# Optimization experiments

Measured on AMD Instinct MI355X. Metric: run time of the kernel, lower is better.

## Reference

```python
import jax, jax.numpy as jnp
import numpy as np

B, T, D, H, K = 128, 64, 2048, 512, 512
WINDOWS = [2, 3, 4]
ROUT = 2 * H            # bidirectional GRU output dim = 1024
FIN = ROUT + len(WINDOWS) * K + 2048 + 1024  # 5632 ('full' concat)
FOUT = 2048
BN_EPS = 1e-5


def setup_inputs() -> dict:
    key = jax.random.key(0)
    ks = jax.random.split(key, 32)
    s = 0.02
    inp = {
        "videos": jax.random.normal(ks[0], (B, T, D), jnp.float32),
        "motions": jax.random.normal(ks[1], (B, 1024), jnp.float32),
        "videos_origin": jax.random.normal(ks[2], (B, 2048), jnp.float32),
        "lengths": jax.random.randint(ks[3], (B,), 1, T + 1, jnp.int32),
        # GRU params (PyTorch layout: gates ordered r,z,n stacked on dim 0)
        "Wih_f": jax.random.normal(ks[4], (3 * H, D), jnp.float32) * s,
        "Whh_f": jax.random.normal(ks[5], (3 * H, H), jnp.float32) * s,
        "bih_f": jnp.zeros((3 * H,), jnp.float32),
        "bhh_f": jnp.zeros((3 * H,), jnp.float32),
        "Wih_b": jax.random.normal(ks[6], (3 * H, D), jnp.float32) * s,
        "Whh_b": jax.random.normal(ks[7], (3 * H, H), jnp.float32) * s,
        "bih_b": jnp.zeros((3 * H,), jnp.float32),
        "bhh_b": jnp.zeros((3 * H,), jnp.float32),
        # FC + BatchNorm1d (eval-mode) of MFC
        "fc_w": jax.random.normal(ks[8], (FOUT, FIN), jnp.float32) * (np.sqrt(6.0) / np.sqrt(FIN + FOUT)),
        "fc_b": jnp.zeros((FOUT,), jnp.float32),
        "bn_gamma": jnp.ones((FOUT,), jnp.float32),
        "bn_beta": jnp.zeros((FOUT,), jnp.float32),
        "bn_mean": jnp.zeros((FOUT,), jnp.float32),
        "bn_var": jnp.ones((FOUT,), jnp.float32),
    }
    for i, ws in enumerate(WINDOWS):
        inp[f"conv_w{ws}"] = jax.random.normal(ks[10 + 2 * i], (K, 1, ws, ROUT), jnp.float32) * s
        inp[f"conv_b{ws}"] = jnp.zeros((K,), jnp.float32)
    # mask consistent with lengths: mask[b,t] = t < lengths[b]
    inp["videos_mask"] = (jnp.arange(T)[None, :] < inp["lengths"][:, None]).astype(jnp.float32)
    return inp


def _gru_dir(x, Wih, Whh, bih, bhh, reverse):
    # x: [B,T,D] -> outputs [B,T,H]; torch GRU cell with r,z,n gate order
    xg = jnp.einsum("btd,gd->btg", x, Wih) + bih  # [B,T,3H] precomputed input gates

    def step(h, xg_t):
        hg = h @ Whh.T + bhh
        xr, xz, xn = jnp.split(xg_t, 3, axis=-1)
        hr, hz, hn = jnp.split(hg, 3, axis=-1)
        r = jax.nn.sigmoid(xr + hr)
        z = jax.nn.sigmoid(xz + hz)
        n = jnp.tanh(xn + r * hn)
        h_new = (1.0 - z) * n + z * h
        return h_new, h_new

    h0 = jnp.zeros((x.shape[0], Whh.shape[1]), x.dtype)
    _, hs = jax.lax.scan(step, h0, jnp.swapaxes(xg, 0, 1), reverse=reverse)
    return jnp.swapaxes(hs, 0, 1)


def _conv_branch(x4, w, b, ws):
    # x4: [B,1,T,ROUT], w: [K,1,ws,ROUT]; torch padding=(ws-1, 0)
    y = jax.lax.conv_general_dilated(
        x4, w, (1, 1), [(ws - 1, ws - 1), (0, 0)],
        dimension_numbers=("NCHW", "OIHW", "NCHW"))  # [B,K,T+ws-1,1]
    y = jax.nn.relu(y + b[None, :, None, None])
    return jnp.max(y, axis=(2, 3))  # max_pool1d over full time -> [B,K]


def _forward(videos, motions, videos_origin, lengths, videos_mask,
             Wih_f, Whh_f, bih_f, bhh_f, Wih_b, Whh_b, bih_b, bhh_b,
             conv_w2, conv_b2, conv_w3, conv_b3, conv_w4, conv_b4,
             fc_w, fc_b, bn_gamma, bn_beta, bn_mean, bn_var):
    fwd = _gru_dir(videos, Wih_f, Whh_f, bih_f, bhh_f, reverse=False)
    bwd = _gru_dir(videos, Wih_b, Whh_b, bih_b, bhh_b, reverse=True)
    gru_init_out = jnp.concatenate([fwd, bwd], axis=-1)  # [B,T,2H]

    # masked mean over valid frames (vectorized version of the batch for-loop)
    denom = lengths.astype(gru_init_out.dtype)[:, None]
    gru_out = jnp.sum(gru_init_out * videos_mask[:, :, None], axis=1) / denom  # [B,2H]

    masked = gru_init_out * videos_mask[:, :, None]
    x4 = masked[:, None, :, :]  # [B,1,T,2H]
    con_out = jnp.concatenate([
        _conv_branch(x4, conv_w2, conv_b2, 2),
        _conv_branch(x4, conv_w3, conv_b3, 3),
        _conv_branch(x4, conv_w4, conv_b4, 4),
    ], axis=1)  # [B,3K]

    # concate == 'full' (dropout is identity in eval)
    features = jnp.concatenate([gru_out, con_out, videos_origin, motions], axis=1)
    features = features @ fc_w.T + fc_b
    # BatchNorm1d, eval mode with running stats
    features = bn_gamma * (features - bn_mean) * jax.lax.rsqrt(bn_var + BN_EPS) + bn_beta
    # l2norm over dim 1
    features = features / jnp.sqrt(jnp.sum(features * features, axis=1, keepdims=True))
    return features


def reference(videos, motions, videos_origin, lengths, videos_mask,
              Wih_f, Whh_f, bih_f, bhh_f, Wih_b, Whh_b, bih_b, bhh_b,
              conv_w2, conv_b2, conv_w3, conv_b3, conv_w4, conv_b4,
              fc_w, fc_b, bn_gamma, bn_beta, bn_mean, bn_var):
    return _forward(videos, motions, videos_origin, lengths, videos_mask,
                    Wih_f, Whh_f, bih_f, bhh_f, Wih_b, Whh_b, bih_b, bhh_b,
                    conv_w2, conv_b2, conv_w3, conv_b3, conv_w4, conv_b4,
                    fc_w, fc_b, bn_gamma, bn_beta, bn_mean, bn_var)
```

## Files before the change

### kernel.cpp

```cpp
#include <hip/hip_runtime.h>
#include <hip/hip_bf16.h>
#include <stdint.h>

typedef __attribute__((ext_vector_type(8))) short short8;
typedef __attribute__((ext_vector_type(4))) float floatx4;
typedef __attribute__((ext_vector_type(4))) unsigned int u32x4;
typedef unsigned short u16;
typedef unsigned int u32;
typedef unsigned long long u64;

static __device__ __forceinline__ u16 f2bf(float f) {
  union { float f; u32 u; } v; v.f = f;
  return (u16)((v.u + 0x7fffu + ((v.u >> 16) & 1u)) >> 16);
}
static __device__ __forceinline__ float bf2f(u16 h) {
  union { u32 u; float f; } v; v.u = ((u32)h) << 16; return v.f;
}
static __device__ __forceinline__ u64 pack4(float a, float b, float c, float d) {
  return (u64)f2bf(a) | ((u64)f2bf(b) << 16) | ((u64)f2bf(c) << 32) | ((u64)f2bf(d) << 48);
}

__global__ __launch_bounds__(256) void k_pre_cvt(
    const float* __restrict__ videos, const float* __restrict__ Wih_f,
    const float* __restrict__ Wih_b, const float* __restrict__ Whh_f,
    const float* __restrict__ Whh_b, const float* __restrict__ bih_f,
    const float* __restrict__ bih_b, const float* __restrict__ fcb,
    const float* __restrict__ gam, const float* __restrict__ bet,
    const float* __restrict__ mu, const float* __restrict__ var,
    u16* __restrict__ vid, u16* __restrict__ wih, u16* __restrict__ whh,
    float* __restrict__ bihcat, float* __restrict__ bns, float* __restrict__ bnt)
{
  const int O1 = 4194304;
  const int O2 = O1 + 786432;
  const int O3 = O2 + 786432;
  const int O4 = O3 + 196608;
  const int O5 = O4 + 196608;
  const int NQ = O5 + 1280;
  for (int q = blockIdx.x * 256 + threadIdx.x; q < NQ; q += gridDim.x * 256) {
    if (q < O1) {
      float4 v = ((const float4*)videos)[q];
      ((u64*)vid)[q] = pack4(v.x, v.y, v.z, v.w);
    } else if (q < O2) {
      int r = q - O1; float4 v = ((const float4*)Wih_f)[r];
      ((u64*)wih)[r] = pack4(v.x, v.y, v.z, v.w);
    } else if (q < O3) {
      int r = q - O2; float4 v = ((const float4*)Wih_b)[r];
      ((u64*)wih)[r + 786432] = pack4(v.x, v.y, v.z, v.w);
    } else if (q < O4) {
      int r = q - O3; float4 v = ((const float4*)Whh_f)[r];
      ((u64*)whh)[r] = pack4(v.x, v.y, v.z, v.w);
    } else if (q < O5) {
      int r = q - O4; float4 v = ((const float4*)Whh_b)[r];
      ((u64*)whh)[r + 196608] = pack4(v.x, v.y, v.z, v.w);
    } else {
      int r = q - O5;
      if (r < 768) {
        int i = r * 4;
        const float* s = (i < 1536) ? (bih_f + i) : (bih_b + (i - 1536));
        *(float4*)&bihcat[i] = *(const float4*)s;
      } else {
        int i = (r - 768) * 4;
#pragma unroll
        for (int j = 0; j < 4; ++j) {
          int idx = i + j;
          float sc = gam[idx] * rsqrtf(var[idx] + 1e-5f);
          bns[idx] = sc;
          bnt[idx] = sc * (fcb[idx] - mu[idx]) + bet[idx];
        }
      }
    }
  }
}

static __device__ __forceinline__ void gload_lds16(const u16* g, u16* l) {
  __builtin_amdgcn_global_load_lds((const __attribute__((address_space(1))) u32*)(const void*)g,
                                   (__attribute__((address_space(3))) u32*)(void*)l, 16, 0, 0);
}

static __device__ __forceinline__ void stage_half_256(
    const u16* __restrict__ Mat, long K, int rowbase, int ktile, u16* lregion,
    int tid, int wid)
{
  int srow = tid >> 3;
  int sce = (((tid >> 3) ^ tid) & 7) * 8;
  const u16* g0 = Mat + (long)(rowbase + srow) * K + ktile * 64 + sce;
  const u16* g1 = Mat + (long)(rowbase + 64 + srow) * K + ktile * 64 + sce;
  gload_lds16(g0, lregion + wid * 512);
  gload_lds16(g1, lregion + 4096 + wid * 512);
}

__global__ __launch_bounds__(512) void gemm256(
    const u16* __restrict__ A, const u16* __restrict__ Bm,
    float* __restrict__ C, u16* __restrict__ C16, int M, int N, int K, int NT,
    const float* __restrict__ shift)
{
  __shared__ u16 lds[65536];
  int tid = threadIdx.x, lane = tid & 63, wid = tid >> 6;
  int r16 = lane & 15, kq = lane >> 4;
  int wr = wid >> 2, wc = wid & 3;
  int nwg = gridDim.x * gridDim.y;
  int lin = blockIdx.y * gridDim.x + blockIdx.x;
  int q8 = nwg >> 3;
  int swz = (lin & 7) * q8 + (lin >> 3);
  int m0 = (swz / gridDim.x) * 256, n0 = (swz % gridDim.x) * 256;

  int fxor = (r16 & 7) << 4;
  int c0 = (kq * 16) ^ fxor;
  int c1 = c0 ^ 64;
  int brow0 = (wc & 1) * 64;
  const char* ldsc = (const char*)lds;

  const floatx4 z4 = {0.f, 0.f, 0.f, 0.f};
  floatx4 acc[8][4];
#pragma unroll
  for (int i = 0; i < 8; ++i)
#pragma unroll
    for (int j = 0; j < 4; ++j) acc[i][j] = z4;

  stage_half_256(Bm, K, n0,       0, lds,                 tid, wid);
  stage_half_256(Bm, K, n0 + 128, 0, lds + 8192,          tid, wid);
  stage_half_256(A,  K, m0,       0, lds + 16384,         tid, wid);
  stage_half_256(A,  K, m0 + 128, 0, lds + 24576,         tid, wid);
  stage_half_256(Bm, K, n0,       1, lds + 32768,         tid, wid);
  stage_half_256(Bm, K, n0 + 128, 1, lds + 32768 + 8192,  tid, wid);
  stage_half_256(A,  K, m0,       1, lds + 32768 + 16384, tid, wid);
  stage_half_256(A,  K, m0 + 128, 1, lds + 32768 + 24576, tid, wid);
  asm volatile("s_waitcnt vmcnt(8)" ::: "memory");
  asm volatile("s_barrier" ::: "memory");

#define MFMA_CLUSTER(q)                                                        \
  asm volatile("s_waitcnt lgkmcnt(0)" ::: "memory");                           \
  __builtin_amdgcn_sched_barrier(0);                                           \
  __builtin_amdgcn_s_setprio(1);                                               \
  _Pragma("unroll")                                                            \
  for (int s = 0; s < 2; ++s)                                                  \
    _Pragma("unroll")                                                          \
    for (int e = 0; e < 2; ++e)                                                \
      _Pragma("unroll")                                                        \
      for (int j = 0; j < 4; ++j)                                              \
        acc[(q)*2 + e][j] = __builtin_amdgcn_mfma_f32_16x16x32_bf16(           \
            af[e][s], bf[j][s], acc[(q)*2 + e][j], 0, 0, 0);                   \
  __builtin_amdgcn_s_setprio(0);

  for (int T = 0; T < NT; ++T) {
    int P = T & 1;
    int Tn1 = (T + 1 < NT) ? T + 1 : 0;
    int Tn2 = (T + 2 < NT) ? T + 2 : T + 2 - NT;
    const char* bbase = ldsc + P * 65536 + (wc >> 1) * 16384;
    const char* abase = ldsc + P * 65536 + 32768 + wr * 16384;
    short8 bf[4][2];
    {
#pragma unroll
      for (int j = 0; j < 4; ++j) {
        bf[j][0] = *(const short8*)(bbase + (brow0 + j * 16 + r16) * 128 + c0);
        bf[j][1] = *(const short8*)(bbase + (brow0 + j * 16 + r16) * 128 + c1);
      }
      short8 af[2][2];
#pragma unroll
      for (int e = 0; e < 2; ++e) {
        af[e][0] = *(const short8*)(abase + (e * 16 + r16) * 128 + c0);
        af[e][1] = *(const short8*)(abase + (e * 16 + r16) * 128 + c1);
      }
      stage_half_256(A, K, m0, Tn1, lds + (Tn1 & 1) * 32768 + 16384, tid, wid);
      asm volatile("s_barrier" ::: "memory");
      MFMA_CLUSTER(0)
      asm volatile("s_barrier" ::: "memory");
    }
    {
      short8 af[2][2];
#pragma unroll
      for (int e = 0; e < 2; ++e) {
        af[e][0] = *(const short8*)(abase + ((2 + e) * 16 + r16) * 128 + c0);
        af[e][1] = *(const short8*)(abase + ((2 + e) * 16 + r16) * 128 + c1);
      }
      stage_half_256(A, K, m0 + 128, Tn1, lds + (Tn1 & 1) * 32768 + 24576, tid, wid);
      asm volatile("s_barrier" ::: "memory");
      MFMA_CLUSTER(1)
      asm volatile("s_barrier" ::: "memory");
    }
    {
      short8 af[2][2];
#pragma unroll
      for (int e = 0; e < 2; ++e) {
        af[e][0] = *(const short8*)(abase + ((4 + e) * 16 + r16) * 128 + c0);
        af[e][1] = *(const short8*)(abase + ((4 + e) * 16 + r16) * 128 + c1);
      }
      stage_half_256(Bm, K, n0, Tn2, lds + P * 32768, tid, wid);
      asm volatile("s_barrier" ::: "memory");
      MFMA_CLUSTER(2)
      asm volatile("s_barrier" ::: "memory");
    }
    {
      short8 af[2][2];
#pragma unroll
      for (int e = 0; e < 2; ++e) {
        af[e][0] = *(const short8*)(abase + ((6 + e) * 16 + r16) * 128 + c0);
        af[e][1] = *(const short8*)(abase + ((6 + e) * 16 + r16) * 128 + c1);
      }
      stage_half_256(Bm, K, n0 + 128, Tn2, lds + P * 32768 + 8192, tid, wid);
      asm volatile("s_barrier" ::: "memory");
      MFMA_CLUSTER(3)
      asm volatile("s_waitcnt vmcnt(4)" ::: "memory");
      asm volatile("s_barrier" ::: "memory");
    }
  }
#undef MFMA_CLUSTER

#pragma unroll
  for (int mf = 0; mf < 8; ++mf)
#pragma unroll
    for (int j = 0; j < 4; ++j) {
      int col = n0 + wc * 64 + j * 16 + r16;
      int row = m0 + wr * 128 + mf * 16 + kq * 4;
      if (C16) {
#pragma unroll
        for (int qq = 0; qq < 4; ++qq)
          C16[(long)(row + qq) * N + col] = f2bf(acc[mf][j][qq]);
      } else {
        float sh = shift ? shift[col] : 0.f;
#pragma unroll
        for (int qq = 0; qq < 4; ++qq)
          C[(long)(row + qq) * N + col] = acc[mf][j][qq] + sh;
      }
    }
}

__global__ __launch_bounds__(256) void gemm_bt(
    const u16* __restrict__ A, const u16* __restrict__ Bm,
    float* __restrict__ C, u16* __restrict__ C16, int M, int N, int K, int kn,
    const float* __restrict__ scale, const float* __restrict__ shift)
{
  __shared__ u16 As[128 * 32];
  __shared__ u16 Bs[128 * 32];
  int tid = threadIdx.x, lane = tid & 63, wid = tid >> 6;
  int nwg = gridDim.x * gridDim.y;
  int lin = blockIdx.y * gridDim.x + blockIdx.x;
  int q8 = nwg >> 3;
  int swz = (lin & 7) * q8 + (lin >> 3);
  int m0 = (swz / gridDim.x) * 128, n0 = (swz % gridDim.x) * 128;
  int kt0 = blockIdx.z * kn;
  int wr = wid >> 1, wc = wid & 1;
  int r16 = lane & 15, kq = lane >> 4;
  const floatx4 z4 = {0.f, 0.f, 0.f, 0.f};
  floatx4 acc[4][4];
#pragma unroll
  for (int i = 0; i < 4; ++i)
#pragma unroll
    for (int j = 0; j < 4; ++j) acc[i][j] = z4;
  for (int kt = kt0; kt < kt0 + kn; ++kt) {
    __syncthreads();
#pragma unroll
    for (int inst = 0; inst < 2; ++inst) {
      int g = inst * 256 + tid;
      int row = g >> 2, cb = g & 3;
      const u16* ga = A + (long)(m0 + row) * K + kt * 32 + cb * 8;
      const u16* gb = Bm + (long)(n0 + row) * K + kt * 32 + cb * 8;
      gload_lds16(ga, &As[(inst * 256 + wid * 64) * 8]);
      gload_lds16(gb, &Bs[(inst * 256 + wid * 64) * 8]);
    }
    __syncthreads();
    short8 af[4], bf[4];
#pragma unroll
    for (int mt = 0; mt < 4; ++mt) af[mt] = *(const short8*)&As[(wr * 64 + mt * 16 + r16) * 32 + kq * 8];
#pragma unroll
    for (int nt = 0; nt < 4; ++nt) bf[nt] = *(const short8*)&Bs[(wc * 64 + nt * 16 + r16) * 32 + kq * 8];
#pragma unroll
    for (int mt = 0; mt < 4; ++mt)
#pragma unroll
      for (int nt = 0; nt < 4; ++nt)
        acc[mt][nt] = __builtin_amdgcn_mfma_f32_16x16x32_bf16(af[mt], bf[nt], acc[mt][nt], 0, 0, 0);
  }
  float* Cp = C + (long)blockIdx.z * M * N;
#pragma unroll
  for (int nt = 0; nt < 4; ++nt) {
    int col = n0 + wc * 64 + nt * 16 + r16;
    float sc = scale ? scale[col] : 1.f;
    float sh = shift ? shift[col] : 0.f;
#pragma unroll
    for (int mt = 0; mt < 4; ++mt)
#pragma unroll
      for (int q = 0; q < 4; ++q) {
        int row = m0 + wr * 64 + mt * 16 + kq * 4 + q;
        float v = acc[mt][nt][q] * sc + sh;
        if (C16) C16[(long)row * N + col] = f2bf(v);
        else     Cp[(long)row * N + col] = v;
      }
  }
}

__global__ __launch_bounds__(512) void gru_rec(
    const float* __restrict__ xg,
    const u16* __restrict__ whhb,
    const float* __restrict__ bhh_f, const float* __restrict__ bhh_b,
    char* __restrict__ hb3,
    u16* __restrict__ maskb,
    u16* __restrict__ feat,
    const int* __restrict__ lengths,
    const float* __restrict__ fc_w, const float* __restrict__ w2,
    const float* __restrict__ w3, const float* __restrict__ w4,
    const float* __restrict__ vo, const float* __restrict__ mo,
    u16* __restrict__ fcw, u16* __restrict__ wc)
{
  __shared__ float part[2][4][3][256];
  __shared__ u16 hstage[8192];
  int tid = threadIdx.x, lane = tid & 63, wid = tid >> 6;
  int bid = blockIdx.x;

  if (bid >= 128) {
    int cid = bid - 128;
    const int C1 = 2883584;
    const int C2 = C1 + 1179648;
    const int C3 = C2 + 65536;
    const int NQ = C3 + 32768;
    for (int q = cid * 512 + tid; q < NQ; q += 128 * 512) {
      if (q < C1) {
        float4 v = ((const float4*)fc_w)[q];
        ((u64*)fcw)[q] = pack4(v.x, v.y, v.z, v.w);
      } else if (q < C2) {
        int r = q - C1;
        int e = r << 2;
        int row = e >> 10, col = e & 1023;
        const float* src;
        if (row < 1024)      { int j = row >> 9, k = row & 511;                 src = w2 + (k * 2 + j) * 1024; }
        else if (row < 2560) { int m = row - 1024; int j = m >> 9, k = m & 511; src = w3 + (k * 3 + j) * 1024; }
        else                 { int m = row - 2560; int j = m >> 9, k = m & 511; src = w4 + (k * 4 + j) * 1024; }
        float4 v = *(const float4*)(src + col);
        ((u64*)wc)[r] = pack4(v.x, v.y, v.z, v.w);
      } else if (q < C3) {
        int r = q - C2; int b = r >> 9, c = (r & 511) * 4;
        float4 v = *(const float4*)&vo[(long)b * 2048 + c];
        *(u64*)&feat[(long)b * 5632 + 2560 + c] = pack4(v.x, v.y, v.z, v.w);
      } else {
        int r = q - C3; int b = r >> 8, c = (r & 255) * 4;
        float4 v = *(const float4*)&mo[(long)b * 1024 + c];
        *(u64*)&feat[(long)b * 5632 + 4608 + c] = pack4(v.x, v.y, v.z, v.w);
      }
    }
    return;
  }

  int dir = bid >> 6, rem = bid & 63, bt = rem >> 3, is = rem & 7;
  int ih = wid & 3, ks = wid >> 2;
  int r16 = lane & 15, kq = lane >> 4;
  int iglob = is * 64 + ih * 16 + r16;
  int i0 = is * 64 + ih * 16 + kq * 4;
  int batch = bt * 16 + r16;
  const float* bhh = dir ? bhh_b : bhh_f;
  const floatx4 z4 = {0.f, 0.f, 0.f, 0.f};
  int len = lengths[batch];

  short8 wfrag[3][8];
#pragma unroll
  for (int g = 0; g < 3; ++g) {
    const u16* wrow = whhb + (long)(dir * 1536 + g * 512 + iglob) * 512;
#pragma unroll
    for (int kk = 0; kk < 8; ++kk)
      wfrag[g][kk] = *(const short8*)&wrow[(ks * 8 + kk) * 32 + kq * 8];
  }
  float4 bh4[3];
#pragma unroll
  for (int g = 0; g < 3; ++g) bh4[g] = *(const float4*)&bhh[g * 512 + i0];
  float4 hprev = {0.f, 0.f, 0.f, 0.f};
  float4 msum = {0.f, 0.f, 0.f, 0.f};

  float4 px[3];
  if (ks == 0) {
    int ts0 = dir ? 63 : 0;
    long xb = (long)(batch * 64 + ts0) * 3072 + dir * 1536 + i0;
#pragma unroll
    for (int g = 0; g < 3; ++g) px[g] = *(const float4*)&xg[xb + g * 512];
  }

  char* slot[2];
  slot[0] = hb3 + (long)((0 * 2 + dir) * 8 + bt) * 32768;
  slot[1] = hb3 + (long)((1 * 2 + dir) * 8 + bt) * 32768;
  char* sdst[4];
#pragma unroll
  for (int k = 0; k < 4; ++k) {
    int row = 4 * k + (tid >> 7);
    int colb = (tid & 127) * 8;
    sdst[k] = (char*)hstage + row * 1024 + (colb ^ ((row & 7) << 4));
  }
  int ld_off = tid * 16;
  int p0 = r16 * 256 + is * 32 + ih * 8 + kq * 2;
  int rb = r16 * 1024 + ks * 512 + kq * 16;
  int rsw = (r16 & 7) << 4;

  for (int t = 0; t < 64; ++t) {
    int par = t & 1;
    u32 tg = (u32)t;
    const char* sb = slot[par];
    u32x4 L0, L1, L2, L3;
    while (true) {
      asm volatile(
        "global_load_dwordx4 %0, %4, off sc0 sc1\n\t"
        "global_load_dwordx4 %1, %5, off sc0 sc1\n\t"
        "global_load_dwordx4 %2, %6, off sc0 sc1\n\t"
        "global_load_dwordx4 %3, %7, off sc0 sc1\n\t"
        "s_waitcnt vmcnt(0)"
        : "=&v"(L0), "=&v"(L1), "=&v"(L2), "=&v"(L3)
        : "v"(sb + ld_off), "v"(sb + 8192 + ld_off),
          "v"(sb + 16384 + ld_off), "v"(sb + 24576 + ld_off)
        : "memory");
      bool ok = (L0.y == tg) & (L0.w == tg) & (L1.y == tg) & (L1.w == tg) &
                (L2.y == tg) & (L2.w == tg) & (L3.y == tg) & (L3.w == tg);
      if (ok) break;
      __builtin_amdgcn_s_sleep(1);
    }
    *(u64*)sdst[0] = (u64)L0.x | ((u64)L0.z << 32);
    *(u64*)sdst[1] = (u64)L1.x | ((u64)L1.z << 32);
    *(u64*)sdst[2] = (u64)L2.x | ((u64)L2.z << 32);
    *(u64*)sdst[3] = (u64)L3.x | ((u64)L3.z << 32);
    float4 pxn[3];
    if (ks == 0 && t < 63) {
      int ts1 = dir ? (62 - t) : (t + 1);
      long xb = (long)(batch * 64 + ts1) * 3072 + dir * 1536 + i0;
#pragma unroll
      for (int g = 0; g < 3; ++g) pxn[g] = *(const float4*)&xg[xb + g * 512];
    }
    asm volatile("s_waitcnt lgkmcnt(0)\n\ts_barrier" ::: "memory");
    floatx4 acc[3];
#pragma unroll
    for (int g = 0; g < 3; ++g) acc[g] = z4;
#pragma unroll
    for (int kk = 0; kk < 8; ++kk) {
      short8 hv = *(const short8*)((const char*)hstage + ((rb + kk * 64) ^ rsw));
#pragma unroll
      for (int g = 0; g < 3; ++g)
        acc[g] = __builtin_amdgcn_mfma_f32_16x16x32_bf16(wfrag[g][kk], hv, acc[g], 0, 0, 0);
    }
    if (ks == 1) {
#pragma unroll
      for (int g = 0; g < 3; ++g) *(floatx4*)&part[par][ih][g][lane * 4] = acc[g];
    }
    asm volatile("s_waitcnt lgkmcnt(0)\n\ts_barrier" ::: "memory");
    if (ks == 0) {
      int tsrc = dir ? (63 - t) : t;
#pragma unroll
      for (int g = 0; g < 3; ++g) acc[g] += *(const floatx4*)&part[par][ih][g][lane * 4];
      float4 hn4;
#pragma unroll
      for (int q = 0; q < 4; ++q) {
        float rr = acc[0][q] + ((const float*)&bh4[0])[q] + ((const float*)&px[0])[q];
        float zz = acc[1][q] + ((const float*)&bh4[1])[q] + ((const float*)&px[1])[q];
        float r = 1.f / (1.f + __expf(-rr));
        float z = 1.f / (1.f + __expf(-zz));
        float n = tanhf(((const float*)&px[2])[q] + r * (acc[2][q] + ((const float*)&bh4[2])[q]));
        ((float*)&hn4)[q] = (1.f - z) * n + z * ((const float*)&hprev)[q];
      }
      hprev = hn4;
      u64 hval = pack4(hn4.x, hn4.y, hn4.z, hn4.w);
      if (t < 63) {
        u32 tg1 = (u32)(t + 1);
        char* pb = slot[(t + 1) & 1] + p0 * 8;
        u64 v0 = (u64)(u32)hval | ((u64)tg1 << 32);
        u64 v1 = (u64)(u32)(hval >> 32) | ((u64)tg1 << 32);
        asm volatile("global_atomic_swap_x2 %0, %1, off sc1"
                     :: "v"(pb), "v"(v0) : "memory");
        asm volatile("global_atomic_swap_x2 %0, %1, off sc1"
                     :: "v"(pb + 8), "v"(v1) : "memory");
      }
      bool mv = tsrc < len;
      *(u64*)&maskb[(long)(batch * 64 + tsrc) * 1024 + dir * 512 + i0] = mv ? hval : 0ull;
      if (mv) {
        msum.x += hn4.x; msum.y += hn4.y; msum.z += hn4.z; msum.w += hn4.w;
      }
      px[0] = pxn[0]; px[1] = pxn[1]; px[2] = pxn[2];
    }
  }
  if (ks == 0) {
    float inv = 1.0f / (float)len;
    *(u64*)&feat[(long)batch * 5632 + dir * 512 + i0] =
        pack4(msum.x * inv, msum.y * inv, msum.z * inv, msum.w * inv);
  }
}

__global__ __launch_bounds__(256) void k_conv_finish(
    const u16* __restrict__ z, const float* __restrict__ cb2,
    const float* __restrict__ cb3, const float* __restrict__ cb4,
    u16* __restrict__ feat)
{
  int b = blockIdx.x, wsi = blockIdx.y, k2 = threadIdx.x * 2;
  int ws = wsi + 2;
  int base = (wsi == 0) ? 0 : (wsi == 1 ? 1024 : 2560);
  const float* cb = (wsi == 0) ? cb2 : (wsi == 1 ? cb3 : cb4);
  float bias0 = cb[k2], bias1 = cb[k2 + 1];
  float m0 = 0.f, m1 = 0.f;
  for (int p = 0; p < 64 + ws - 1; ++p) {
    float a0 = bias0, a1 = bias1;
    for (int j = 0; j < ws; ++j) {
      int t = p - (ws - 1) + j;
      if (t >= 0 && t < 64) {
        u32 v = *(const u32*)&z[(long)(b * 64 + t) * 4608 + base + j * 512 + k2];
        a0 += bf2f((u16)v);
        a1 += bf2f((u16)(v >> 16));
      }
    }
    m0 = fmaxf(m0, a0);
    m1 = fmaxf(m1, a1);
  }
  *(u32*)&feat[(long)b * 5632 + 1024 + wsi * 512 + k2] = (u32)f2bf(m0) | ((u32)f2bf(m1) << 16);
}

__global__ __launch_bounds__(256) void k_l2norm(const float* __restrict__ p,
    const float* __restrict__ bns, const float* __restrict__ bnt, float* __restrict__ out)
{
  __shared__ float red[4];
  int b = blockIdx.x, tid = threadIdx.x;
  float v[8]; float s = 0.f;
#pragma unroll
  for (int j = 0; j < 8; ++j) {
    int i = j * 256 + tid;
    long o = (long)b * 2048 + i;
    float a = 0.f;
#pragma unroll
    for (int zz = 0; zz < 8; ++zz) a += p[o + (long)zz * 262144];
    a = a * bns[i] + bnt[i];
    v[j] = a; s += a * a;
  }
#pragma unroll
  for (int o = 32; o > 0; o >>= 1) s += __shfl_down(s, o);
  if ((tid & 63) == 0) red[tid >> 6] = s;
  __syncthreads();
  float rn = rsqrtf(red[0] + red[1] + red[2] + red[3]);
#pragma unroll
  for (int j = 0; j < 8; ++j)
    out[(long)b * 2048 + j * 256 + tid] = v[j] * rn;
}

extern "C" void kernel_launch(void* const* d_in, const int* in_sizes, int n_in,
                              void* d_out, int out_size, void* d_ws, size_t ws_size,
                              hipStream_t stream)
{
  (void)in_sizes; (void)n_in; (void)out_size; (void)ws_size;
  const float* videos       = (const float*)d_in[0];
  const float* motions      = (const float*)d_in[1];
  const float* videos_origin= (const float*)d_in[2];
  const int*   lengths      = (const int*)d_in[3];
  const float* Wih_f = (const float*)d_in[4];
  const float* Whh_f = (const float*)d_in[5];
  const float* bih_f = (const float*)d_in[6];
  const float* bhh_f = (const float*)d_in[7];
  const float* Wih_b = (const float*)d_in[8];
  const float* Whh_b = (const float*)d_in[9];
  const float* bih_b = (const float*)d_in[10];
  const float* bhh_b = (const float*)d_in[11];
  const float* fc_w  = (const float*)d_in[12];
  const float* fc_b  = (const float*)d_in[13];
  const float* bn_gamma = (const float*)d_in[14];
  const float* bn_beta  = (const float*)d_in[15];
  const float* bn_mean  = (const float*)d_in[16];
  const float* bn_var   = (const float*)d_in[17];
  const float* conv_w2 = (const float*)d_in[18];
  const float* conv_b2 = (const float*)d_in[19];
  const float* conv_w3 = (const float*)d_in[20];
  const float* conv_b3 = (const float*)d_in[21];
  const float* conv_w4 = (const float*)d_in[22];
  const float* conv_b4 = (const float*)d_in[23];
  float* out = (float*)d_out;
  char* w = (char*)d_ws;

  const size_t XG    = 0;
  const size_t HS    = 100663296;
  const size_t VID   = 134217728;
  const size_t MASKB = 167772160;
  const size_t WIH   = 184549376;
  const size_t WHH   = 197132288;
  const size_t WC    = 200278016;
  const size_t FCW   = 209715200;
  const size_t FEAT  = 232783872;
  const size_t BIH   = 235274240;
  const size_t BNS   = 235286528;
  const size_t BNT   = 235294720;

  float* xg   = (float*)(w + XG);
  u16*   zb16 = (u16*)(w + XG);
  char* hb3   = (char*)(w + HS);
  u16* vid    = (u16*)(w + VID);
  u16* maskb  = (u16*)(w + MASKB);
  float* fcp  = (float*)(w + MASKB);
  u16* wih    = (u16*)(w + WIH);
  u16* whh    = (u16*)(w + WHH);
  u16* wc_    = (u16*)(w + WC);
  u16* fcw    = (u16*)(w + FCW);
  u16* feat   = (u16*)(w + FEAT);
  float* bih  = (float*)(w + BIH);
  float* bns  = (float*)(w + BNS);
  float* bnt  = (float*)(w + BNT);

  hipMemsetAsync(hb3, 0, 1048576, stream);

  k_pre_cvt<<<4096, 256, 0, stream>>>(
      videos, Wih_f, Wih_b, Whh_f, Whh_b, bih_f, bih_b,
      fc_b, bn_gamma, bn_beta, bn_mean, bn_var,
      vid, wih, whh, bih, bns, bnt);

  gemm256<<<dim3(12, 32), 512, 0, stream>>>(vid, wih, xg, nullptr, 8192, 3072, 2048, 32, bih);

  {
    const float* xg_c = xg; const u16* whh_c = whh;
    char* hb_c = hb3; u16* mb_c = maskb; u16* ft_c = feat;
    const int* len_c = lengths;
    const float* bf_c = bhh_f; const float* bb_c = bhh_b;
    const float* fw_c = fc_w; const float* w2_c = conv_w2;
    const float* w3_c = conv_w3; const float* w4_c = conv_w4;
    const float* vo_c = videos_origin; const float* mo_c = motions;
    u16* fcw_c = fcw; u16* wc_c = wc_;
    void* args[] = { (void*)&xg_c, (void*)&whh_c, (void*)&bf_c, (void*)&bb_c,
                     (void*)&hb_c, (void*)&mb_c, (void*)&ft_c, (void*)&len_c,
                     (void*)&fw_c, (void*)&w2_c, (void*)&w3_c, (void*)&w4_c,
                     (void*)&vo_c, (void*)&mo_c, (void*)&fcw_c, (void*)&wc_c };
    hipLaunchCooperativeKernel(reinterpret_cast<void*>(gru_rec), dim3(256), dim3(512), args, 0, stream);
  }

  gemm256<<<dim3(18, 32), 512, 0, stream>>>(maskb, wc_, nullptr, zb16, 8192, 4608, 1024, 16, nullptr);
  k_conv_finish<<<dim3(128, 3), 256, 0, stream>>>(zb16, conv_b2, conv_b3, conv_b4, feat);
  gemm_bt<<<dim3(16, 1, 8), 256, 0, stream>>>(feat, fcw, fcp, nullptr, 128, 2048, 5632, 22, nullptr, nullptr);
  k_l2norm<<<128, 256, 0, stream>>>(fcp, bns, bnt, out);
}
```

Baseline: 560.5 us.

## Fuse conv window-sum and max-pool epilogue into conv GEMM via LDS

The conv GEMM now keeps its 256x256 output tile in LDS and performs the per-window shifted sums, bias add and temporal max-pool directly, writing pooled features to the concat buffer. This removes the bf16 intermediate Z round trip through global memory and the separate finish kernel. To make each tile self-contained, conv weight rows are re-laid out interleaved by tap (window-3 padded to 4 taps), growing N from 4608 to 5120 with some wasted MFMA work. The epilogue pooling uses only a fraction of the threads and runs serially per tile.

```diff
diff --git a/kernel.cpp b/kernel.cpp
--- a/kernel.cpp
+++ b/kernel.cpp
@@ -89,44 +89,99 @@
   gload_lds16(g1, lregion + 4096 + wid * 512);
 }
 
-__global__ __launch_bounds__(512) void gemm256(
-    const u16* __restrict__ A, const u16* __restrict__ Bm,
-    float* __restrict__ C, u16* __restrict__ C16, int M, int N, int K, int NT,
-    const float* __restrict__ shift)
-{
-  __shared__ u16 lds[65536];
-  int tid = threadIdx.x, lane = tid & 63, wid = tid >> 6;
-  int r16 = lane & 15, kq = lane >> 4;
-  int wr = wid >> 2, wc = wid & 3;
-  int nwg = gridDim.x * gridDim.y;
-  int lin = blockIdx.y * gridDim.x + blockIdx.x;
-  int q8 = nwg >> 3;
-  int swz = (lin & 7) * q8 + (lin >> 3);
-  int m0 = (swz / gridDim.x) * 256, n0 = (swz % gridDim.x) * 256;
-
-  int fxor = (r16 & 7) << 4;
-  int c0 = (kq * 16) ^ fxor;
-  int c1 = c0 ^ 64;
-  int brow0 = (wc & 1) * 64;
-  const char* ldsc = (const char*)lds;
-
-  const floatx4 z4 = {0.f, 0.f, 0.f, 0.f};
-  floatx4 acc[8][4];
-#pragma unroll
-  for (int i = 0; i < 8; ++i)
-#pragma unroll
-    for (int j = 0; j < 4; ++j) acc[i][j] = z4;
-
-  stage_half_256(Bm, K, n0,       0, lds,                 tid, wid);
-  stage_half_256(Bm, K, n0 + 128, 0, lds + 8192,          tid, wid);
-  stage_half_256(A,  K, m0,       0, lds + 16384,         tid, wid);
-  stage_half_256(A,  K, m0 + 128, 0, lds + 24576,         tid, wid);
-  stage_half_256(Bm, K, n0,       1, lds + 32768,         tid, wid);
-  stage_half_256(Bm, K, n0 + 128, 1, lds + 32768 + 8192,  tid, wid);
-  stage_half_256(A,  K, m0,       1, lds + 32768 + 16384, tid, wid);
-  stage_half_256(A,  K, m0 + 128, 1, lds + 32768 + 24576, tid, wid);
-  asm volatile("s_waitcnt vmcnt(8)" ::: "memory");
-  asm volatile("s_barrier" ::: "memory");
+#define GEMM256_BODY(A, Bm, K, NT)                                             \
+  __shared__ u16 lds[65536];                                                   \
+  int tid = threadIdx.x, lane = tid & 63, wid = tid >> 6;                      \
+  int r16 = lane & 15, kq = lane >> 4;                                         \
+  int wr = wid >> 2, wc = wid & 3;                                             \
+  int nwg = gridDim.x * gridDim.y;                                             \
+  int lin = blockIdx.y * gridDim.x + blockIdx.x;                               \
+  int q8 = nwg >> 3;                                                           \
+  int swz = (lin & 7) * q8 + (lin >> 3);                                       \
+  int m0 = (swz / gridDim.x) * 256, n0 = (swz % gridDim.x) * 256;              \
+  int fxor = (r16 & 7) << 4;                                                   \
+  int c0 = (kq * 16) ^ fxor;                                                   \
+  int c1 = c0 ^ 64;                                                            \
+  int brow0 = (wc & 1) * 64;                                                   \
+  const char* ldsc = (const char*)lds;                                         \
+  const floatx4 z4 = {0.f, 0.f, 0.f, 0.f};                                     \
+  floatx4 acc[8][4];                                                           \
+  _Pragma("unroll")                                                            \
+  for (int i = 0; i < 8; ++i)                                                  \
+    _Pragma("unroll")                                                          \
+    for (int j = 0; j < 4; ++j) acc[i][j] = z4;                                \
+  stage_half_256(Bm, K, n0,       0, lds,                 tid, wid);           \
+  stage_half_256(Bm, K, n0 + 128, 0, lds + 8192,          tid, wid);           \
+  stage_half_256(A,  K, m0,       0, lds + 16384,         tid, wid);           \
+  stage_half_256(A,  K, m0 + 128, 0, lds + 24576,         tid, wid);           \
+  stage_half_256(Bm, K, n0,       1, lds + 32768,         tid, wid);           \
+  stage_half_256(Bm, K, n0 + 128, 1, lds + 32768 + 8192,  tid, wid);           \
+  stage_half_256(A,  K, m0,       1, lds + 32768 + 16384, tid, wid);           \
+  stage_half_256(A,  K, m0 + 128, 1, lds + 32768 + 24576, tid, wid);           \
+  asm volatile("s_waitcnt vmcnt(8)" ::: "memory");                             \
+  asm volatile("s_barrier" ::: "memory");                                      \
+  for (int T = 0; T < NT; ++T) {                                               \
+    int P = T & 1;                                                             \
+    int Tn1 = (T + 1 < NT) ? T + 1 : 0;                                        \
+    int Tn2 = (T + 2 < NT) ? T + 2 : T + 2 - NT;                               \
+    const char* bbase = ldsc + P * 65536 + (wc >> 1) * 16384;                  \
+    const char* abase = ldsc + P * 65536 + 32768 + wr * 16384;                 \
+    short8 bf[4][2];                                                           \
+    {                                                                          \
+      _Pragma("unroll")                                                        \
+      for (int j = 0; j < 4; ++j) {                                            \
+        bf[j][0] = *(const short8*)(bbase + (brow0 + j * 16 + r16) * 128 + c0);\
+        bf[j][1] = *(const short8*)(bbase + (brow0 + j * 16 + r16) * 128 + c1);\
+      }                                                                        \
+      short8 af[2][2];                                                         \
+      _Pragma("unroll")                                                        \
+      for (int e = 0; e < 2; ++e) {                                            \
+        af[e][0] = *(const short8*)(abase + (e * 16 + r16) * 128 + c0);        \
+        af[e][1] = *(const short8*)(abase + (e * 16 + r16) * 128 + c1);        \
+      }                                                                        \
+      stage_half_256(A, K, m0, Tn1, lds + (Tn1 & 1) * 32768 + 16384, tid, wid);\
+      asm volatile("s_barrier" ::: "memory");                                  \
+      MFMA_CLUSTER(0)                                                          \
+      asm volatile("s_barrier" ::: "memory");                                  \
+    }                                                                          \
+    {                                                                          \
+      short8 af[2][2];                                                         \
+      _Pragma("unroll")                                                        \
+      for (int e = 0; e < 2; ++e) {                                            \
+        af[e][0] = *(const short8*)(abase + ((2 + e) * 16 + r16) * 128 + c0);  \
+        af[e][1] = *(const short8*)(abase + ((2 + e) * 16 + r16) * 128 + c1);  \
+      }                                                                        \
+      stage_half_256(A, K, m0 + 128, Tn1, lds + (Tn1 & 1) * 32768 + 24576, tid, wid); \
+      asm volatile("s_barrier" ::: "memory");                                  \
+      MFMA_CLUSTER(1)                                                          \
+      asm volatile("s_barrier" ::: "memory");                                  \
+    }                                                                          \
+    {                                                                          \
+      short8 af[2][2];                                                         \
+      _Pragma("unroll")                                                        \
+      for (int e = 0; e < 2; ++e) {                                            \
+        af[e][0] = *(const short8*)(abase + ((4 + e) * 16 + r16) * 128 + c0);  \
+        af[e][1] = *(const short8*)(abase + ((4 + e) * 16 + r16) * 128 + c1);  \
+      }                                                                        \
+      stage_half_256(Bm, K, n0, Tn2, lds + P * 32768, tid, wid);               \
+      asm volatile("s_barrier" ::: "memory");                                  \
+      MFMA_CLUSTER(2)                                                          \
+      asm volatile("s_barrier" ::: "memory");                                  \
+    }                                                                          \
+    {                                                                          \
+      short8 af[2][2];                                                         \
+      _Pragma("unroll")                                                        \
+      for (int e = 0; e < 2; ++e) {                                            \
+        af[e][0] = *(const short8*)(abase + ((6 + e) * 16 + r16) * 128 + c0);  \
+        af[e][1] = *(const short8*)(abase + ((6 + e) * 16 + r16) * 128 + c1);  \
+      }                                                                        \
+      stage_half_256(Bm, K, n0 + 128, Tn2, lds + P * 32768 + 8192, tid, wid);  \
+      asm volatile("s_barrier" ::: "memory");                                  \
+      MFMA_CLUSTER(3)                                                          \
+      asm volatile("s_waitcnt vmcnt(4)" ::: "memory");                         \
+      asm volatile("s_barrier" ::: "memory");                                  \
+    }                                                                          \
+  }
 
 #define MFMA_CLUSTER(q)                                                        \
   asm volatile("s_waitcnt lgkmcnt(0)" ::: "memory");                           \
@@ -142,93 +197,75 @@
             af[e][s], bf[j][s], acc[(q)*2 + e][j], 0, 0, 0);                   \
   __builtin_amdgcn_s_setprio(0);
 
-  for (int T = 0; T < NT; ++T) {
-    int P = T & 1;
-    int Tn1 = (T + 1 < NT) ? T + 1 : 0;
-    int Tn2 = (T + 2 < NT) ? T + 2 : T + 2 - NT;
-    const char* bbase = ldsc + P * 65536 + (wc >> 1) * 16384;
-    const char* abase = ldsc + P * 65536 + 32768 + wr * 16384;
-    short8 bf[4][2];
-    {
-#pragma unroll
-      for (int j = 0; j < 4; ++j) {
-        bf[j][0] = *(const short8*)(bbase + (brow0 + j * 16 + r16) * 128 + c0);
-        bf[j][1] = *(const short8*)(bbase + (brow0 + j * 16 + r16) * 128 + c1);
-      }
-      short8 af[2][2];
-#pragma unroll
-      for (int e = 0; e < 2; ++e) {
-        af[e][0] = *(const short8*)(abase + (e * 16 + r16) * 128 + c0);
-        af[e][1] = *(const short8*)(abase + (e * 16 + r16) * 128 + c1);
-      }
-      stage_half_256(A, K, m0, Tn1, lds + (Tn1 & 1) * 32768 + 16384, tid, wid);
-      asm volatile("s_barrier" ::: "memory");
-      MFMA_CLUSTER(0)
-      asm volatile("s_barrier" ::: "memory");
-    }
-    {
-      short8 af[2][2];
-#pragma unroll
-      for (int e = 0; e < 2; ++e) {
-        af[e][0] = *(const short8*)(abase + ((2 + e) * 16 + r16) * 128 + c0);
-        af[e][1] = *(const short8*)(abase + ((2 + e) * 16 + r16) * 128 + c1);
-      }
-      stage_half_256(A, K, m0 + 128, Tn1, lds + (Tn1 & 1) * 32768 + 24576, tid, wid);
-      asm volatile("s_barrier" ::: "memory");
-      MFMA_CLUSTER(1)
-      asm volatile("s_barrier" ::: "memory");
-    }
-    {
-      short8 af[2][2];
-#pragma unroll
-      for (int e = 0; e < 2; ++e) {
-        af[e][0] = *(const short8*)(abase + ((4 + e) * 16 + r16) * 128 + c0);
-        af[e][1] = *(const short8*)(abase + ((4 + e) * 16 + r16) * 128 + c1);
-      }
-      stage_half_256(Bm, K, n0, Tn2, lds + P * 32768, tid, wid);
-      asm volatile("s_barrier" ::: "memory");
-      MFMA_CLUSTER(2)
-      asm volatile("s_barrier" ::: "memory");
-    }
-    {
-      short8 af[2][2];
-#pragma unroll
-      for (int e = 0; e < 2; ++e) {
-        af[e][0] = *(const short8*)(abase + ((6 + e) * 16 + r16) * 128 + c0);
-        af[e][1] = *(const short8*)(abase + ((6 + e) * 16 + r16) * 128 + c1);
-      }
-      stage_half_256(Bm, K, n0 + 128, Tn2, lds + P * 32768 + 8192, tid, wid);
-      asm volatile("s_barrier" ::: "memory");
-      MFMA_CLUSTER(3)
-      asm volatile("s_waitcnt vmcnt(4)" ::: "memory");
-      asm volatile("s_barrier" ::: "memory");
-    }
-  }
-#undef MFMA_CLUSTER
-
+__global__ __launch_bounds__(512) void gemm256(
+    const u16* __restrict__ A, const u16* __restrict__ Bm,
+    float* __restrict__ C, int N, int K, int NT,
+    const float* __restrict__ shift)
+{
+  GEMM256_BODY(A, Bm, K, NT)
 #pragma unroll
   for (int mf = 0; mf < 8; ++mf)
 #pragma unroll
     for (int j = 0; j < 4; ++j) {
       int col = n0 + wc * 64 + j * 16 + r16;
       int row = m0 + wr * 128 + mf * 16 + kq * 4;
-      if (C16) {
-#pragma unroll
-        for (int qq = 0; qq < 4; ++qq)
-          C16[(long)(row + qq) * N + col] = f2bf(acc[mf][j][qq]);
-      } else {
-        float sh = shift ? shift[col] : 0.f;
-#pragma unroll
-        for (int qq = 0; qq < 4; ++qq)
-          C[(long)(row + qq) * N + col] = acc[mf][j][qq] + sh;
+      float sh = shift ? shift[col] : 0.f;
+#pragma unroll
+      for (int qq = 0; qq < 4; ++qq)
+        C[(long)(row + qq) * N + col] = acc[mf][j][qq] + sh;
+    }
+}
+
+__global__ __launch_bounds__(512) void gemm256c(
+    const u16* __restrict__ A, const u16* __restrict__ Bm,
+    u16* __restrict__ feat, const float* __restrict__ cb2,
+    const float* __restrict__ cb3, const float* __restrict__ cb4,
+    int K, int NT)
+{
+  GEMM256_BODY(A, Bm, K, NT)
+  asm volatile("s_waitcnt vmcnt(0)" ::: "memory");
+  asm volatile("s_barrier" ::: "memory");
+  u16* zt = lds;
+#pragma unroll
+  for (int mf = 0; mf < 8; ++mf)
+#pragma unroll
+    for (int j = 0; j < 4; ++j) {
+      int col = wc * 64 + j * 16 + r16;
+      int row = wr * 128 + mf * 16 + kq * 4;
+#pragma unroll
+      for (int qq = 0; qq < 4; ++qq)
+        zt[(row + qq) * 256 + col] = f2bf(acc[mf][j][qq]);
+    }
+  __syncthreads();
+  int S, k0, fo, ws;
+  const float* cb;
+  if (n0 < 1024)      { S = 2; k0 = n0 >> 1;          cb = cb2; fo = 1024; ws = 2; }
+  else if (n0 < 3072) { S = 4; k0 = (n0 - 1024) >> 2; cb = cb3; fo = 1536; ws = 3; }
+  else                { S = 4; k0 = (n0 - 3072) >> 2; cb = cb4; fo = 2048; ws = 4; }
+  int KT = 256 / S;
+  if (tid < 4 * KT) {
+    int b = tid / KT, kk = tid % KT;
+    float bias = cb[k0 + kk];
+    float m = 0.f;
+    for (int p = 0; p < 64 + ws - 1; ++p) {
+      float a = bias;
+      for (int j = 0; j < ws; ++j) {
+        int t = p - (ws - 1) + j;
+        if (t >= 0 && t < 64)
+          a += bf2f(zt[(b * 64 + t) * 256 + kk * S + j]);
       }
-    }
-}
+      m = fmaxf(m, a);
+    }
+    int gb = (m0 >> 6) + b;
+    feat[(long)gb * 5632 + fo + k0 + kk] = f2bf(m);
+  }
+}
+#undef MFMA_CLUSTER
+#undef GEMM256_BODY
 
 __global__ __launch_bounds__(256) void gemm_bt(
     const u16* __restrict__ A, const u16* __restrict__ Bm,
-    float* __restrict__ C, u16* __restrict__ C16, int M, int N, int K, int kn,
-    const float* __restrict__ scale, const float* __restrict__ shift)
+    float* __restrict__ C, int M, int N, int K, int kn)
 {
   __shared__ u16 As[128 * 32];
   __shared__ u16 Bs[128 * 32];
@@ -274,16 +311,12 @@
 #pragma unroll
   for (int nt = 0; nt < 4; ++nt) {
     int col = n0 + wc * 64 + nt * 16 + r16;
-    float sc = scale ? scale[col] : 1.f;
-    float sh = shift ? shift[col] : 0.f;
 #pragma unroll
     for (int mt = 0; mt < 4; ++mt)
 #pragma unroll
       for (int q = 0; q < 4; ++q) {
         int row = m0 + wr * 64 + mt * 16 + kq * 4 + q;
-        float v = acc[mt][nt][q] * sc + sh;
-        if (C16) C16[(long)row * N + col] = f2bf(v);
-        else     Cp[(long)row * N + col] = v;
+        Cp[(long)row * N + col] = acc[mt][nt][q];
       }
   }
 }
@@ -309,7 +342,7 @@
   if (bid >= 128) {
     int cid = bid - 128;
     const int C1 = 2883584;
-    const int C2 = C1 + 1179648;
+    const int C2 = C1 + 1310720;
     const int C3 = C2 + 65536;
     const int NQ = C3 + 32768;
     for (int q = cid * 512 + tid; q < NQ; q += 128 * 512) {
@@ -320,11 +353,13 @@
         int r = q - C1;
         int e = r << 2;
         int row = e >> 10, col = e & 1023;
-        const float* src;
-        if (row < 1024)      { int j = row >> 9, k = row & 511;                 src = w2 + (k * 2 + j) * 1024; }
-        else if (row < 2560) { int m = row - 1024; int j = m >> 9, k = m & 511; src = w3 + (k * 3 + j) * 1024; }
-        else                 { int m = row - 2560; int j = m >> 9, k = m & 511; src = w4 + (k * 4 + j) * 1024; }
-        float4 v = *(const float4*)(src + col);
+        float4 v = {0.f, 0.f, 0.f, 0.f};
+        if (row < 1024)      { int k = row >> 1, j = row & 1;
+                               v = *(const float4*)(w2 + (k * 2 + j) * 1024 + col); }
+        else if (row < 3072) { int m = row - 1024; int k = m >> 2, j = m & 3;
+                               if (j < 3) v = *(const float4*)(w3 + (k * 3 + j) * 1024 + col); }
+        else                 { int m = row - 3072; int k = m >> 2, j = m & 3;
+                               v = *(const float4*)(w4 + (k * 4 + j) * 1024 + col); }
         ((u64*)wc)[r] = pack4(v.x, v.y, v.z, v.w);
       } else if (q < C3) {
         int r = q - C2; int b = r >> 9, c = (r & 511) * 4;
@@ -473,33 +508,6 @@
     *(u64*)&feat[(long)batch * 5632 + dir * 512 + i0] =
         pack4(msum.x * inv, msum.y * inv, msum.z * inv, msum.w * inv);
   }
-}
-
-__global__ __launch_bounds__(256) void k_conv_finish(
-    const u16* __restrict__ z, const float* __restrict__ cb2,
-    const float* __restrict__ cb3, const float* __restrict__ cb4,
-    u16* __restrict__ feat)
-{
-  int b = blockIdx.x, wsi = blockIdx.y, k2 = threadIdx.x * 2;
-  int ws = wsi + 2;
-  int base = (wsi == 0) ? 0 : (wsi == 1 ? 1024 : 2560);
-  const float* cb = (wsi == 0) ? cb2 : (wsi == 1 ? cb3 : cb4);
-  float bias0 = cb[k2], bias1 = cb[k2 + 1];
-  float m0 = 0.f, m1 = 0.f;
-  for (int p = 0; p < 64 + ws - 1; ++p) {
-    float a0 = bias0, a1 = bias1;
-    for (int j = 0; j < ws; ++j) {
-      int t = p - (ws - 1) + j;
-      if (t >= 0 && t < 64) {
-        u32 v = *(const u32*)&z[(long)(b * 64 + t) * 4608 + base + j * 512 + k2];
-        a0 += bf2f((u16)v);
-        a1 += bf2f((u16)(v >> 16));
-      }
-    }
-    m0 = fmaxf(m0, a0);
-    m1 = fmaxf(m1, a1);
-  }
-  *(u32*)&feat[(long)b * 5632 + 1024 + wsi * 512 + k2] = (u32)f2bf(m0) | ((u32)f2bf(m1) << 16);
 }
 
 __global__ __launch_bounds__(256) void k_l2norm(const float* __restrict__ p,
@@ -566,7 +574,6 @@
   const size_t MASKB = 167772160;
   const size_t WIH   = 184549376;
   const size_t WHH   = 197132288;
-  const size_t WC    = 200278016;
   const size_t FCW   = 209715200;
   const size_t FEAT  = 232783872;
   const size_t BIH   = 235274240;
@@ -574,14 +581,13 @@
   const size_t BNT   = 235294720;
 
   float* xg   = (float*)(w + XG);
-  u16*   zb16 = (u16*)(w + XG);
   char* hb3   = (char*)(w + HS);
+  u16* wc_    = (u16*)(w + HS + 1048576);
   u16* vid    = (u16*)(w + VID);
   u16* maskb  = (u16*)(w + MASKB);
   float* fcp  = (float*)(w + MASKB);
   u16* wih    = (u16*)(w + WIH);
   u16* whh    = (u16*)(w + WHH);
-  u16* wc_    = (u16*)(w + WC);
   u16* fcw    = (u16*)(w + FCW);
   u16* feat   = (u16*)(w + FEAT);
   float* bih  = (float*)(w + BIH);
@@ -595,7 +601,7 @@
       fc_b, bn_gamma, bn_beta, bn_mean, bn_var,
       vid, wih, whh, bih, bns, bnt);
 
-  gemm256<<<dim3(12, 32), 512, 0, stream>>>(vid, wih, xg, nullptr, 8192, 3072, 2048, 32, bih);
+  gemm256<<<dim3(12, 32), 512, 0, stream>>>(vid, wih, xg, 3072, 2048, 32, bih);
 
   {
     const float* xg_c = xg; const u16* whh_c = whh;
@@ -613,8 +619,7 @@
     hipLaunchCooperativeKernel(reinterpret_cast<void*>(gru_rec), dim3(256), dim3(512), args, 0, stream);
   }
 
-  gemm256<<<dim3(18, 32), 512, 0, stream>>>(maskb, wc_, nullptr, zb16, 8192, 4608, 1024, 16, nullptr);
-  k_conv_finish<<<dim3(128, 3), 256, 0, stream>>>(zb16, conv_b2, conv_b3, conv_b4, feat);
-  gemm_bt<<<dim3(16, 1, 8), 256, 0, stream>>>(feat, fcw, fcp, nullptr, 128, 2048, 5632, 22, nullptr, nullptr);
+  gemm256c<<<dim3(20, 32), 512, 0, stream>>>(maskb, wc_, feat, conv_b2, conv_b3, conv_b4, 1024, 16);
+  gemm_bt<<<dim3(16, 1, 8), 256, 0, stream>>>(feat, fcw, fcp, 128, 2048, 5632, 22);
   k_l2norm<<<128, 256, 0, stream>>>(fcp, bns, bnt, out);
 }
```

Result: faster. 518.6 us (median of 2 runs) (-7.5%).
